# Kernel optimization log

Measured on AMD Instinct MI355X. Metric: run time of the kernel, lower is better.

The kernel has to match this reference:

```python
import jax, jax.numpy as jnp
import numpy as np

C, T, V, H, DQ = 64, 128, 25, 3, 32  # channels, frames, joints, heads, qkv_dim
EPS = 1e-5
LRELU_SLOPE = 0.1


def pos_embed(channels, num_frames, num_joints):
    # DSTA-Net style sinusoidal Pos_Embed: position index is the joint id, tiled over frames
    pos = np.tile(np.arange(num_joints, dtype=np.float32), num_frames)[:, None]  # (T*V, 1)
    div = np.exp(np.arange(0, channels, 2, dtype=np.float32) * -(np.log(10000.0) / channels))
    pe = np.zeros((num_frames * num_joints, channels), dtype=np.float32)
    pe[:, 0::2] = np.sin(pos * div)
    pe[:, 1::2] = np.cos(pos * div)
    pe = pe.reshape(num_frames, num_joints, channels).transpose(2, 0, 1)[None]  # (1, C, T, V)
    return jnp.asarray(pe)


def batchnorm2d(x, gamma, beta):
    # training-mode BN over (N, T, V) per channel, biased variance (torch default)
    m = x.mean(axis=(0, 2, 3), keepdims=True)
    v = x.var(axis=(0, 2, 3), keepdims=True)
    return (x - m) * jax.lax.rsqrt(v + EPS) * gamma[None, :, None, None] + beta[None, :, None, None]


def setup_inputs() -> dict:
    key = jax.random.key(0)
    ks = jax.random.split(key, 4)
    N = 64
    return {
        "x": jax.random.normal(ks[0], (N, C, T, V), jnp.float32),
        "Wqkv": jax.random.normal(ks[1], (2 * H * DQ, C), jnp.float32) * 0.05,   # 1x1 conv weight
        "bqkv": jnp.zeros((2 * H * DQ,), jnp.float32),
        "alphas": jnp.ones((1, H, 1, 1), jnp.float32),
        "att0s": jax.random.uniform(ks[2], (1, H, V, V), jnp.float32) / V,
        "Wout": jax.random.normal(ks[3], (C, H * C, 1, 5), jnp.float32) * 0.02,  # (1,5) temporal conv
        "bout": jnp.zeros((C,), jnp.float32),
        "gamma": jnp.ones((C,), jnp.float32),
        "beta": jnp.zeros((C,), jnp.float32),
    }


def reference(x, Wqkv, bqkv, alphas, att0s, Wout, bout, gamma, beta):
    N = x.shape[0]
    xs = x + pos_embed(C, T, V)                                   # pes(x) + x
    qk = jnp.einsum('nctv,oc->notv', xs, Wqkv) + bqkv[None, :, None, None]
    qk = qk.reshape(N, 2 * H, DQ, T, V)
    q, k = qk[:, :H], qk[:, H:]
    # tanh-gated joint-attention, no softmax
    att = jnp.tanh(jnp.einsum('nhctu,nhctv->nhuv', q, k) / (DQ * T)) * alphas + att0s
    y = jnp.einsum('nctu,nhuv->nhctv', x, att).reshape(N, H * C, T, V)
    y = jax.lax.conv_general_dilated(
        y, Wout, window_strides=(1, 1), padding=((0, 0), (2, 2)),
        dimension_numbers=('NCHW', 'OIHW', 'NCHW')) + bout[None, :, None, None]
    y = batchnorm2d(y, gamma, beta)
    return jax.nn.leaky_relu(y + x, LRELU_SLOPE)                  # ress is identity (in==out)
```

## Files before the change

kernel.cpp:

```cpp
#include <hip/hip_runtime.h>
#include <hip/hip_bf16.h>


#define WS_ATT   0
#define WS_STATS 120000
#define WS_WBF   120128
#define WS_WP    150848
#define WS_BP    156992
#define WS_PE    157184

typedef __attribute__((ext_vector_type(8))) short short8;
typedef __attribute__((ext_vector_type(4))) float floatx4;

__device__ __forceinline__ float us2f(unsigned short u) {
    union { unsigned int i; float f; } w; w.i = ((unsigned int)u) << 16; return w.f;
}
__device__ __forceinline__ unsigned short f2us(float f) {
    __hip_bfloat16_raw r = __float2bfloat16(f); return r.x;
}

__device__ __forceinline__ int swz(int col, int byteoff) {
    return col * 128 + ((((byteoff >> 4) ^ (col & 7)) << 4) | (byteoff & 15));
}

__device__ __forceinline__ void bar_lgkm() {
    asm volatile("s_waitcnt lgkmcnt(0)" ::: "memory");
    __builtin_amdgcn_s_barrier();
}

__global__ void k_wprep(const float* __restrict__ Wout, const float* __restrict__ Wqkv,
                        const float* __restrict__ bqkv, unsigned short* __restrict__ Abf,
                        unsigned short* __restrict__ Wp, float* __restrict__ bp,
                        float* __restrict__ pe)
{
    int i = blockIdx.x * 256 + threadIdx.x;
    if (i < 61440) {
        int tap = i / 12288, rem = i % 12288;
        int o = rem / 192, hc = rem % 192;
        Abf[i] = f2us(Wout[o * 960 + hc * 5 + tap]);
    } else if (i < 73728) {
        int j = i - 61440;
        int np = j >> 6, c = j & 63;
        int h = np >> 6, qk = (np >> 5) & 1, cp = np & 31;
        Wp[j] = f2us(Wqkv[(qk * 96 + h * 32 + cp) * 64 + c]);
    } else if (i < 73920) {
        int np = i - 73728;
        int h = np >> 6, qk = (np >> 5) & 1, cp = np & 31;
        bp[np] = bqkv[qk * 96 + h * 32 + cp];
    } else if (i < 75520) {
        int e = i - 73920;
        int c = e / 25, v = e % 25;
        int ii = c >> 1;
        float d = expf(-(float)(2 * ii) * (9.210340371976184f / 64.0f));
        float a = (float)v * d;
        pe[e] = (c & 1) ? cosf(a) : sinf(a);
    }
}

#define CPAD 112

__global__ __launch_bounds__(256, 2) void k_att(
    const float* __restrict__ x, const unsigned short* __restrict__ Wp,
    const float* __restrict__ bp, const float* __restrict__ peg,
    float* __restrict__ att_raw)
{
    __shared__ unsigned short xs_s[2][CPAD * 64];
    __shared__ unsigned short qk_s[3 * CPAD * 64];
    __shared__ float pe_s[1600];

    const int tid  = threadIdx.x;
    const int lane = tid & 63, wv = tid >> 6;
    const int l16  = lane & 15, quad = lane >> 4;
    const int n    = blockIdx.y;
    const int tb0  = blockIdx.x * 16;

    const int col_a = lane;
    const int col_b = 64 + lane;
    const int va = (col_a < 25) ? col_a : (col_a < 50 ? col_a - 25 : col_a - 50);
    const int vb = (col_b < 75) ? col_b - 50 : col_b - 75;
    char* qkb = (char*)qk_s;

    float ra0[8], ra1[8], rb0[8], rb1[8];

#define LOADCH(CH) do {                                                         \
    const int g0_ = (tb0 + (CH) * 4) * 25;                                      \
    _Pragma("unroll")                                                           \
    for (int cp8 = 0; cp8 < 8; ++cp8) {                                         \
        const float* xp0_ = x + (size_t)(n * 64 + (wv * 8 + cp8) * 2) * 3200 + g0_; \
        const float* xp1_ = xp0_ + 3200;                                        \
        ra0[cp8] = xp0_[col_a]; ra1[cp8] = xp1_[col_a];                         \
        if (lane < 36) { rb0[cp8] = xp0_[col_b]; rb1[cp8] = xp1_[col_b]; }      \
    } } while (0)

    LOADCH(0);

    for (int e = tid; e < 1600; e += 256) pe_s[e] = peg[e];

    short8 afrag[3][2];
    float  biasr[3][4];
    #pragma unroll
    for (int mt = 0; mt < 3; ++mt) {
        int row = (3 * wv + mt) * 16 + l16;
        #pragma unroll
        for (int kk = 0; kk < 2; ++kk)
            afrag[mt][kk] = *(const short8*)(Wp + row * 64 + kk * 32 + quad * 8);
        #pragma unroll
        for (int reg = 0; reg < 4; ++reg)
            biasr[mt][reg] = bp[(3 * wv + mt) * 16 + quad * 4 + reg];
    }

    floatx4 qacc[3][2][2];
    #pragma unroll
    for (int h = 0; h < 3; ++h)
        #pragma unroll
        for (int a = 0; a < 2; ++a)
            #pragma unroll
            for (int b = 0; b < 2; ++b)
                qacc[h][a][b] = (floatx4){0.0f, 0.0f, 0.0f, 0.0f};

    bar_lgkm();

    #pragma unroll
    for (int ch = 0; ch < 4; ++ch) {
        char* xsb = (char*)xs_s[ch & 1];

        #pragma unroll
        for (int cp8 = 0; cp8 < 8; ++cp8) {
            const int cpair = wv * 8 + cp8, c0 = cpair * 2;
            unsigned int pk =
                (unsigned int)f2us(ra0[cp8] + pe_s[c0 * 25 + va]) |
                ((unsigned int)f2us(ra1[cp8] + pe_s[c0 * 25 + 25 + va]) << 16);
            *(unsigned int*)(xsb + swz(col_a, cpair * 4)) = pk;
            if (lane < 36) {
                pk = (unsigned int)f2us(rb0[cp8] + pe_s[c0 * 25 + vb]) |
                     ((unsigned int)f2us(rb1[cp8] + pe_s[c0 * 25 + 25 + vb]) << 16);
                *(unsigned int*)(xsb + swz(col_b, cpair * 4)) = pk;
            }
        }
        if (ch < 3) LOADCH(ch + 1);
        bar_lgkm();

        #pragma unroll
        for (int nt = 0; nt < 7; ++nt) {
            const int col = nt * 16 + l16;
            short8 b0 = *(const short8*)(xsb + swz(col, quad * 16));
            short8 b1 = *(const short8*)(xsb + swz(col, 64 + quad * 16));
            #pragma unroll
            for (int mt = 0; mt < 3; ++mt) {
                floatx4 acc = (floatx4){0.0f, 0.0f, 0.0f, 0.0f};
                acc = __builtin_amdgcn_mfma_f32_16x16x32_bf16(afrag[mt][0], b0, acc, 0, 0, 0);
                acc = __builtin_amdgcn_mfma_f32_16x16x32_bf16(afrag[mt][1], b1, acc, 0, 0, 0);
                const int np  = (3 * wv + mt) * 16 + quad * 4;
                const int h   = np >> 6;
                const int off = (np & 63) * 2;
                unsigned long long pk =
                      (unsigned long long)f2us(acc[0] + biasr[mt][0])
                    | ((unsigned long long)f2us(acc[1] + biasr[mt][1]) << 16)
                    | ((unsigned long long)f2us(acc[2] + biasr[mt][2]) << 32)
                    | ((unsigned long long)f2us(acc[3] + biasr[mt][3]) << 48);
                *(unsigned long long*)(qkb + h * (CPAD * 128) + swz(col, off)) = pk;
            }
        }
        bar_lgkm();

        const int tcol = wv * 25;
        #pragma unroll
        for (int h = 0; h < 3; ++h) {
            char* qh = qkb + h * (CPAD * 128);
            short8 qa0 = *(const short8*)(qh + swz(tcol + l16,      quad * 16));
            short8 qa1 = *(const short8*)(qh + swz(tcol + 16 + l16, quad * 16));
            short8 kb0 = *(const short8*)(qh + swz(tcol + l16,      64 + quad * 16));
            short8 kb1 = *(const short8*)(qh + swz(tcol + 16 + l16, 64 + quad * 16));
            qacc[h][0][0] = __builtin_amdgcn_mfma_f32_16x16x32_bf16(qa0, kb0, qacc[h][0][0], 0, 0, 0);
            qacc[h][0][1] = __builtin_amdgcn_mfma_f32_16x16x32_bf16(qa0, kb1, qacc[h][0][1], 0, 0, 0);
            qacc[h][1][0] = __builtin_amdgcn_mfma_f32_16x16x32_bf16(qa1, kb0, qacc[h][1][0], 0, 0, 0);
            qacc[h][1][1] = __builtin_amdgcn_mfma_f32_16x16x32_bf16(qa1, kb1, qacc[h][1][1], 0, 0, 0);
        }
    }

    __syncthreads();
    float* att_s = (float*)qk_s;
    for (int e = tid; e < 1875; e += 256) att_s[e] = 0.0f;
    __syncthreads();
    #pragma unroll
    for (int h = 0; h < 3; ++h) {
        #pragma unroll
        for (int ut = 0; ut < 2; ++ut) {
            #pragma unroll
            for (int vt = 0; vt < 2; ++vt) {
                const int v = vt * 16 + l16;
                if (v < 25) {
                    const int ub = ut * 16 + quad * 4;
                    #pragma unroll
                    for (int reg = 0; reg < 4; ++reg) {
                        const int u = ub + reg;
                        if (u < 25)
                            atomicAdd(&att_s[h * 625 + u * 25 + v], qacc[h][ut][vt][reg]);
                    }
                }
            }
        }
    }
    __syncthreads();
    for (int e = tid; e < 1875; e += 256)
        atomicAdd(&att_raw[(size_t)n * 1875 + e], att_s[e]);
}

__global__ void k_attfin(float* __restrict__ att, const float* __restrict__ alphas,
                         const float* __restrict__ att0s)
{
    int idx = blockIdx.x * 256 + threadIdx.x;
    if (idx >= 64 * 3 * 625) return;
    int nh = idx / 625, p = idx % 625;
    int h = nh % 3;
    float a = att[idx];
    att[idx] = tanhf(a * (1.0f / 4096.0f)) * alphas[h] + att0s[h * 625 + p];
}

__global__ __launch_bounds__(256, 3) void k_conv(
    const float* __restrict__ x, const unsigned short* __restrict__ Abf,
    const float* __restrict__ bout, const float* __restrict__ att,
    float* __restrict__ out)
{
    __shared__ unsigned short yT[11136];
    __shared__ unsigned short x_sb[4096];
    __shared__ unsigned short attT[3000];

    const int tid = threadIdx.x;
    const int n = blockIdx.y;
    const int t0 = blockIdx.x * 2;
    char* xsb = (char*)x_sb;

    for (int e = tid; e < 896; e += 256) {
        int c = e / 14, r = e % 14;
        int t = r / 7, u = 25 + r % 7;
        *(unsigned short*)(xsb + swz(c, (t * 32 + u) * 2)) = 0;
    }
    for (int e = tid; e < 1125; e += 256) {
        int rv = e / 15, u = 25 + e % 15;
        attT[rv * 40 + u] = 0;
    }
    for (int e = tid; e < 1600; e += 256) {
        int c = e / 25, j = e % 25;
        const float2 xv = *(const float2*)(x + (size_t)(n * 64 + c) * 3200 + t0 * 25 + 2 * j);
        int i0 = 2 * j, i1 = i0 + 1;
        int p0 = (i0 / 25) * 32 + (i0 % 25);
        int p1 = (i1 / 25) * 32 + (i1 % 25);
        *(unsigned short*)(xsb + swz(c, p0 * 2)) = f2us(xv.x);
        *(unsigned short*)(xsb + swz(c, p1 * 2)) = f2us(xv.y);
    }
    for (int e = tid; e < 1875; e += 256) {
        int h = e / 625, r = e % 625, u = r / 25, v = r % 25;
        attT[(h * 25 + v) * 40 + u] = f2us(att[n * 1875 + e]);
    }
    for (int e = tid; e < 1536; e += 256) {
        int t = e / 768, r = e % 768;
        int vi = r / 192, hc = r % 192;
        int vv = (vi < 2) ? vi : (25 + vi);
        int phys = (t * 29 + vv) * 192 + (((hc >> 3) ^ (vv & 7)) << 3) + (hc & 7);
        yT[phys] = 0;
    }
    __syncthreads();

    const int lane = tid & 63, wv = tid >> 6;
    const int quad = lane >> 4, l16 = lane & 15;

    {
        const int c0 = wv * 16;
        const int crow = c0 + l16;
        short8 af[2];
        #pragma unroll
        for (int t = 0; t < 2; ++t)
            af[t] = *(const short8*)(xsb + swz(crow, (t * 32 + quad * 8) * 2));
        short8 bfr[3][2];
        #pragma unroll
        for (int h = 0; h < 3; ++h)
            #pragma unroll
            for (int nt = 0; nt < 2; ++nt) {
                int v = nt * 16 + l16; if (v > 24) v = 24;
                bfr[h][nt] = *(const short8*)&attT[(h * 25 + v) * 40 + quad * 8];
            }
        #pragma unroll
        for (int t = 0; t < 2; ++t)
            #pragma unroll
            for (int h = 0; h < 3; ++h)
                #pragma unroll
                for (int nt = 0; nt < 2; ++nt) {
                    floatx4 d = (floatx4){0.0f, 0.0f, 0.0f, 0.0f};
                    d = __builtin_amdgcn_mfma_f32_16x16x32_bf16(af[t], bfr[h][nt], d, 0, 0, 0);
                    const int v = nt * 16 + l16;
                    if (v < 25) {
                        const int vv = v + 2;
                        const int hc = h * 64 + c0 + quad * 4;
                        const int phys = (t * 29 + vv) * 192 + (((hc >> 3) ^ (vv & 7)) << 3) + (hc & 7);
                        unsigned long long pk =
                              (unsigned long long)f2us(d[0])
                            | ((unsigned long long)f2us(d[1]) << 16)
                            | ((unsigned long long)f2us(d[2]) << 32)
                            | ((unsigned long long)f2us(d[3]) << 48);
                        *(unsigned long long*)&yT[phys] = pk;
                    }
                }
    }

    const int o0 = wv * 16;
    short8 areg[5][6];
    const unsigned short* apb = Abf + (o0 + l16) * 192 + quad * 8;
    #pragma unroll
    for (int tap = 0; tap < 5; ++tap)
        #pragma unroll
        for (int kk = 0; kk < 6; ++kk)
            areg[tap][kk] = *(const short8*)(apb + tap * 12288 + kk * 32);
    float bo[4];
    #pragma unroll
    for (int reg = 0; reg < 4; ++reg) bo[reg] = bout[o0 + quad * 4 + reg];

    bar_lgkm();

    #pragma unroll
    for (int nt = 0; nt < 4; ++nt) {
        int col = nt * 16 + l16;
        const bool ok = col < 50;
        if (col > 49) col = 49;
        const int tc = col / 25, vc = col % 25;
        floatx4 acc = (floatx4){0.0f, 0.0f, 0.0f, 0.0f};
        #pragma unroll
        for (int tap = 0; tap < 5; ++tap) {
            const int vv = vc + tap;
            const int ro = (tc * 29 + vv) * 192, vx = vv & 7;
            #pragma unroll
            for (int kk = 0; kk < 6; ++kk) {
                short8 b = *(const short8*)&yT[ro + (((kk * 4 + quad) ^ vx) << 3)];
                acc = __builtin_amdgcn_mfma_f32_16x16x32_bf16(areg[tap][kk], b, acc, 0, 0, 0);
            }
        }
        if (ok) {
            float* op = out + (size_t)(n * 64 + o0 + quad * 4) * 3200 + (t0 + tc) * 25 + vc;
            #pragma unroll
            for (int reg = 0; reg < 4; ++reg)
                op[(size_t)reg * 3200] = acc[reg] + bo[reg];
        }
    }
}

__global__ __launch_bounds__(256) void k_stats(const float* __restrict__ conv,
                                               float* __restrict__ stats)
{
    const int o = blockIdx.y;
    const int n0 = blockIdx.x * 8;
    const int tid = threadIdx.x;
    float s1 = 0.0f, s2 = 0.0f;
    for (int e = tid; e < 8 * 3200; e += 256) {
        int nl = e / 3200, i = e % 3200;
        float v = conv[(size_t)((n0 + nl) * 64 + o) * 3200 + i];
        s1 += v; s2 = fmaf(v, v, s2);
    }
    for (int off = 32; off > 0; off >>= 1) {
        s1 += __shfl_down(s1, off);
        s2 += __shfl_down(s2, off);
    }
    __shared__ float r1[4], r2[4];
    int w = tid >> 6;
    if ((tid & 63) == 0) { r1[w] = s1; r2[w] = s2; }
    __syncthreads();
    if (tid == 0) {
        atomicAdd(&stats[o],      r1[0] + r1[1] + r1[2] + r1[3]);
        atomicAdd(&stats[64 + o], r2[0] + r2[1] + r2[2] + r2[3]);
    }
}

__global__ void k_final(const float* __restrict__ stats, const float4* __restrict__ x4,
                        const float* __restrict__ gamma, const float* __restrict__ beta,
                        float4* __restrict__ out4)
{
    int idx = blockIdx.x * 256 + threadIdx.x;
    if (idx >= 3276800) return;
    int o = (idx / 800) & 63;
    const float inv = 1.0f / 204800.0f;
    float m   = stats[o] * inv;
    float ex2 = stats[64 + o] * inv;
    float var = ex2 - m * m;
    float r = rsqrtf(var + 1e-5f);
    float g = gamma[o], bb = beta[o];
    float4 v = out4[idx];
    float4 xx = x4[idx];
    float4 res;
    float t;
    t = (v.x - m) * r * g + bb + xx.x; res.x = fmaxf(t, 0.1f * t);
    t = (v.y - m) * r * g + bb + xx.y; res.y = fmaxf(t, 0.1f * t);
    t = (v.z - m) * r * g + bb + xx.z; res.z = fmaxf(t, 0.1f * t);
    t = (v.w - m) * r * g + bb + xx.w; res.w = fmaxf(t, 0.1f * t);
    out4[idx] = res;
}

extern "C" void kernel_launch(void* const* d_in, const int* in_sizes, int n_in,
                              void* d_out, int out_size, void* d_ws, size_t ws_size,
                              hipStream_t stream)
{
    const float* x      = (const float*)d_in[0];
    const float* Wqkv   = (const float*)d_in[1];
    const float* bqkv   = (const float*)d_in[2];
    const float* alphas = (const float*)d_in[3];
    const float* att0s  = (const float*)d_in[4];
    const float* Wout   = (const float*)d_in[5];
    const float* bout   = (const float*)d_in[6];
    const float* gamma  = (const float*)d_in[7];
    const float* beta   = (const float*)d_in[8];
    float* ws  = (float*)d_ws;
    float* out = (float*)d_out;
    unsigned short* Abf = (unsigned short*)(ws + WS_WBF);
    unsigned short* Wp  = (unsigned short*)(ws + WS_WP);
    float*          bp  = ws + WS_BP;
    float*          pe  = ws + WS_PE;

    hipMemsetAsync(d_ws, 0, (size_t)(120000 + 128) * sizeof(float), stream);

    k_wprep <<<296, 256, 0, stream>>>(Wout, Wqkv, bqkv, Abf, Wp, bp, pe);
    k_att   <<<dim3(8, 64),  256, 0, stream>>>(x, Wp, bp, pe, ws + WS_ATT);
    k_attfin<<<(120000 + 255) / 256, 256, 0, stream>>>(ws + WS_ATT, alphas, att0s);
    k_conv  <<<dim3(64, 64), 256, 0, stream>>>(x, Abf, bout, ws + WS_ATT, out);
    k_stats <<<dim3(8, 64),  256, 0, stream>>>(out, ws + WS_STATS);
    k_final <<<12800,        256, 0, stream>>>(ws + WS_STATS, (const float4*)x,
                                               gamma, beta, (float4*)out);
}
```

Measured before the change: 302.5 us.

## Fuse BN statistics into conv epilogue and pre-transpose attention to bf16

Result: slower. 395.2 us (+30.6%).

```diff
diff --git a/kernel.cpp b/kernel.cpp
--- a/kernel.cpp
+++ b/kernel.cpp
@@ -2,12 +2,14 @@
 #include <hip/hip_bf16.h>
 
 
-#define WS_ATT   0
-#define WS_STATS 120000
-#define WS_WBF   120128
-#define WS_WP    150848
-#define WS_BP    156992
-#define WS_PE    157184
+#define WS_ATT    0
+#define WS_STATS  120000
+#define WS_WBF    120128
+#define WS_WP     150848
+#define WS_BP     156992
+#define WS_PE     157184
+#define WS_SPART  158784
+#define WS_ATTBF  166976
 
 typedef __attribute__((ext_vector_type(8))) short short8;
 typedef __attribute__((ext_vector_type(4))) float floatx4;
@@ -206,39 +208,49 @@
         atomicAdd(&att_raw[(size_t)n * 1875 + e], att_s[e]);
 }
 
-__global__ void k_attfin(float* __restrict__ att, const float* __restrict__ alphas,
+__global__ void k_attfin(const float* __restrict__ att_raw,
+                         unsigned short* __restrict__ attbf,
+                         const float* __restrict__ alphas,
                          const float* __restrict__ att0s)
 {
     int idx = blockIdx.x * 256 + threadIdx.x;
-    if (idx >= 64 * 3 * 625) return;
-    int nh = idx / 625, p = idx % 625;
+    if (idx >= 64 * 3 * 25 * 40) return;
+    int u = idx % 40;
+    int r = idx / 40;
+    int v = r % 25;
+    int nh = r / 25;
     int h = nh % 3;
-    float a = att[idx];
-    att[idx] = tanhf(a * (1.0f / 4096.0f)) * alphas[h] + att0s[h * 625 + p];
-}
-
-__global__ __launch_bounds__(256, 3) void k_conv(
+    unsigned short val = 0;
+    if (u < 25) {
+        float a = att_raw[nh * 625 + u * 25 + v];
+        val = f2us(tanhf(a * (1.0f / 4096.0f)) * alphas[h] + att0s[h * 625 + u * 25 + v]);
+    }
+    attbf[idx] = val;
+}
+
+__global__ __launch_bounds__(256, 4) void k_conv(
     const float* __restrict__ x, const unsigned short* __restrict__ Abf,
-    const float* __restrict__ bout, const float* __restrict__ att,
-    float* __restrict__ out)
+    const float* __restrict__ bout, const unsigned short* __restrict__ attbf,
+    float* __restrict__ out, float* __restrict__ spart)
 {
     __shared__ unsigned short yT[11136];
     __shared__ unsigned short x_sb[4096];
     __shared__ unsigned short attT[3000];
+    __shared__ float bout_s[64];
+    __shared__ float stats_s[128];
 
     const int tid = threadIdx.x;
     const int n = blockIdx.y;
     const int t0 = blockIdx.x * 2;
     char* xsb = (char*)x_sb;
 
+    if (tid < 128) stats_s[tid] = 0.0f;
+    if (tid < 64)  bout_s[tid] = bout[tid];
+
     for (int e = tid; e < 896; e += 256) {
         int c = e / 14, r = e % 14;
         int t = r / 7, u = 25 + r % 7;
         *(unsigned short*)(xsb + swz(c, (t * 32 + u) * 2)) = 0;
-    }
-    for (int e = tid; e < 1125; e += 256) {
-        int rv = e / 15, u = 25 + e % 15;
-        attT[rv * 40 + u] = 0;
     }
     for (int e = tid; e < 1600; e += 256) {
         int c = e / 25, j = e % 25;
@@ -249,9 +261,10 @@
         *(unsigned short*)(xsb + swz(c, p0 * 2)) = f2us(xv.x);
         *(unsigned short*)(xsb + swz(c, p1 * 2)) = f2us(xv.y);
     }
-    for (int e = tid; e < 1875; e += 256) {
-        int h = e / 625, r = e % 625, u = r / 25, v = r % 25;
-        attT[(h * 25 + v) * 40 + u] = f2us(att[n * 1875 + e]);
+    {
+        const uint4* src = (const uint4*)(attbf + (size_t)n * 3000);
+        uint4* dst = (uint4*)attT;
+        for (int e = tid; e < 375; e += 256) dst[e] = src[e];
     }
     for (int e = tid; e < 1536; e += 256) {
         int t = e / 768, r = e % 768;
@@ -303,70 +316,74 @@
                 }
     }
 
-    const int o0 = wv * 16;
-    short8 areg[5][6];
-    const unsigned short* apb = Abf + (o0 + l16) * 192 + quad * 8;
+    bar_lgkm();
+
+    const int col = wv * 16 + l16;
+    const bool ok = col < 50;
+    const int colc = ok ? col : 49;
+    const int tc = colc / 25, vc = colc % 25;
+
+    floatx4 acc0 = {0,0,0,0}, acc1 = {0,0,0,0}, acc2 = {0,0,0,0}, acc3 = {0,0,0,0};
+    const unsigned short* apb = Abf + l16 * 192 + quad * 8;
+
     #pragma unroll
-    for (int tap = 0; tap < 5; ++tap)
-        #pragma unroll
-        for (int kk = 0; kk < 6; ++kk)
-            areg[tap][kk] = *(const short8*)(apb + tap * 12288 + kk * 32);
-    float bo[4];
-    #pragma unroll
-    for (int reg = 0; reg < 4; ++reg) bo[reg] = bout[o0 + quad * 4 + reg];
-
-    bar_lgkm();
-
-    #pragma unroll
-    for (int nt = 0; nt < 4; ++nt) {
-        int col = nt * 16 + l16;
-        const bool ok = col < 50;
-        if (col > 49) col = 49;
-        const int tc = col / 25, vc = col % 25;
-        floatx4 acc = (floatx4){0.0f, 0.0f, 0.0f, 0.0f};
-        #pragma unroll
-        for (int tap = 0; tap < 5; ++tap) {
-            const int vv = vc + tap;
-            const int ro = (tc * 29 + vv) * 192, vx = vv & 7;
-            #pragma unroll
-            for (int kk = 0; kk < 6; ++kk) {
-                short8 b = *(const short8*)&yT[ro + (((kk * 4 + quad) ^ vx) << 3)];
-                acc = __builtin_amdgcn_mfma_f32_16x16x32_bf16(areg[tap][kk], b, acc, 0, 0, 0);
-            }
+    for (int tap = 0; tap < 5; ++tap) {
+        const int vv = vc + tap;
+        const int ro = (tc * 29 + vv) * 192, vx = vv & 7;
+        #pragma unroll
+        for (int kk = 0; kk < 6; ++kk) {
+            short8 b = *(const short8*)&yT[ro + (((kk * 4 + quad) ^ vx) << 3)];
+            const unsigned short* ap = apb + tap * 12288 + kk * 32;
+            acc0 = __builtin_amdgcn_mfma_f32_16x16x32_bf16(*(const short8*)(ap),        b, acc0, 0, 0, 0);
+            acc1 = __builtin_amdgcn_mfma_f32_16x16x32_bf16(*(const short8*)(ap + 3072), b, acc1, 0, 0, 0);
+            acc2 = __builtin_amdgcn_mfma_f32_16x16x32_bf16(*(const short8*)(ap + 6144), b, acc2, 0, 0, 0);
+            acc3 = __builtin_amdgcn_mfma_f32_16x16x32_bf16(*(const short8*)(ap + 9216), b, acc3, 0, 0, 0);
         }
-        if (ok) {
-            float* op = out + (size_t)(n * 64 + o0 + quad * 4) * 3200 + (t0 + tc) * 25 + vc;
-            #pragma unroll
-            for (int reg = 0; reg < 4; ++reg)
-                op[(size_t)reg * 3200] = acc[reg] + bo[reg];
-        }
-    }
-}
-
-__global__ __launch_bounds__(256) void k_stats(const float* __restrict__ conv,
-                                               float* __restrict__ stats)
-{
-    const int o = blockIdx.y;
-    const int n0 = blockIdx.x * 8;
-    const int tid = threadIdx.x;
-    float s1 = 0.0f, s2 = 0.0f;
-    for (int e = tid; e < 8 * 3200; e += 256) {
-        int nl = e / 3200, i = e % 3200;
-        float v = conv[(size_t)((n0 + nl) * 64 + o) * 3200 + i];
-        s1 += v; s2 = fmaf(v, v, s2);
-    }
-    for (int off = 32; off > 0; off >>= 1) {
-        s1 += __shfl_down(s1, off);
-        s2 += __shfl_down(s2, off);
-    }
-    __shared__ float r1[4], r2[4];
-    int w = tid >> 6;
-    if ((tid & 63) == 0) { r1[w] = s1; r2[w] = s2; }
+    }
+
+#define EPIS(ACC, MT)                                                          \
+    do {                                                                       \
+        float vr[4];                                                           \
+        _Pragma("unroll")                                                      \
+        for (int reg = 0; reg < 4; ++reg)                                      \
+            vr[reg] = ok ? ACC[reg] + bout_s[(MT) * 16 + quad * 4 + reg] : 0.0f; \
+        if (ok) {                                                              \
+            float* op = out + (size_t)(n * 64 + (MT) * 16 + quad * 4) * 3200   \
+                        + (t0 + tc) * 25 + vc;                                 \
+            _Pragma("unroll")                                                  \
+            for (int reg = 0; reg < 4; ++reg)                                  \
+                op[(size_t)reg * 3200] = vr[reg];                              \
+        }                                                                      \
+        _Pragma("unroll")                                                      \
+        for (int reg = 0; reg < 4; ++reg) {                                    \
+            float s1 = vr[reg], s2 = vr[reg] * vr[reg];                        \
+            _Pragma("unroll")                                                  \
+            for (int m = 1; m < 16; m <<= 1) {                                 \
+                s1 += __shfl_xor(s1, m);                                       \
+                s2 += __shfl_xor(s2, m);                                       \
+            }                                                                  \
+            if (l16 == 0) {                                                    \
+                atomicAdd(&stats_s[(MT) * 16 + quad * 4 + reg], s1);           \
+                atomicAdd(&stats_s[64 + (MT) * 16 + quad * 4 + reg], s2);      \
+            }                                                                  \
+        }                                                                      \
+    } while (0)
+
+    EPIS(acc0, 0); EPIS(acc1, 1); EPIS(acc2, 2); EPIS(acc3, 3);
+#undef EPIS
+
     __syncthreads();
-    if (tid == 0) {
-        atomicAdd(&stats[o],      r1[0] + r1[1] + r1[2] + r1[3]);
-        atomicAdd(&stats[64 + o], r2[0] + r2[1] + r2[2] + r2[3]);
-    }
+    if (tid < 128)
+        atomicAdd(&spart[(size_t)blockIdx.x * 128 + tid], stats_s[tid]);
+}
+
+__global__ void k_statsred(const float* __restrict__ spart, float* __restrict__ stats)
+{
+    int o = threadIdx.x;
+    float s = 0.0f;
+    #pragma unroll 8
+    for (int t = 0; t < 64; ++t) s += spart[t * 128 + o];
+    stats[o] = s;
 }
 
 __global__ void k_final(const float* __restrict__ stats, const float4* __restrict__ x4,
@@ -408,18 +425,21 @@
     const float* beta   = (const float*)d_in[8];
     float* ws  = (float*)d_ws;
     float* out = (float*)d_out;
-    unsigned short* Abf = (unsigned short*)(ws + WS_WBF);
-    unsigned short* Wp  = (unsigned short*)(ws + WS_WP);
-    float*          bp  = ws + WS_BP;
-    float*          pe  = ws + WS_PE;
-
-    hipMemsetAsync(d_ws, 0, (size_t)(120000 + 128) * sizeof(float), stream);
-
-    k_wprep <<<296, 256, 0, stream>>>(Wout, Wqkv, bqkv, Abf, Wp, bp, pe);
-    k_att   <<<dim3(8, 64),  256, 0, stream>>>(x, Wp, bp, pe, ws + WS_ATT);
-    k_attfin<<<(120000 + 255) / 256, 256, 0, stream>>>(ws + WS_ATT, alphas, att0s);
-    k_conv  <<<dim3(64, 64), 256, 0, stream>>>(x, Abf, bout, ws + WS_ATT, out);
-    k_stats <<<dim3(8, 64),  256, 0, stream>>>(out, ws + WS_STATS);
-    k_final <<<12800,        256, 0, stream>>>(ws + WS_STATS, (const float4*)x,
-                                               gamma, beta, (float4*)out);
-}
+    unsigned short* Abf   = (unsigned short*)(ws + WS_WBF);
+    unsigned short* Wp    = (unsigned short*)(ws + WS_WP);
+    float*          bp    = ws + WS_BP;
+    float*          pe    = ws + WS_PE;
+    float*          spart = ws + WS_SPART;
+    unsigned short* attbf = (unsigned short*)(ws + WS_ATTBF);
+
+    hipMemsetAsync(d_ws, 0, (size_t)120000 * sizeof(float), stream);
+    hipMemsetAsync(spart, 0, (size_t)8192 * sizeof(float), stream);
+
+    k_wprep   <<<296, 256, 0, stream>>>(Wout, Wqkv, bqkv, Abf, Wp, bp, pe);
+    k_att     <<<dim3(8, 64),  256, 0, stream>>>(x, Wp, bp, pe, ws + WS_ATT);
+    k_attfin  <<<750, 256, 0, stream>>>(ws + WS_ATT, attbf, alphas, att0s);
+    k_conv    <<<dim3(64, 64), 256, 0, stream>>>(x, Abf, bout, attbf, out, spart);
+    k_statsred<<<1, 128, 0, stream>>>(spart, ws + WS_STATS);
+    k_final   <<<12800, 256, 0, stream>>>(ws + WS_STATS, (const float4*)x,
+                                          gamma, beta, (float4*)out);
+}
```
